# Performance work log

Hardware: AMD Instinct MI355X
Metric: run time of the kernel (lower is better)

Reference implementation:

```python
import jax, jax.numpy as jnp
import numpy as np

N_NODES = 262144          # 8192 graphs * 32 nodes
N_EDGES = 2097152         # avg degree 8
C_IN = 64
C_HID = 64
C_OUT_GCN = 64            # 'output' layer -> channel_out = 64
NODES_PER_BATCH = 32
FC_IN = NODES_PER_BATCH * C_OUT_GCN   # 2048
FC_HID = 256
OUT_DIM = 32
NEG_SLOPE = 0.2


def setup_inputs() -> dict:
    key = jax.random.key(0)
    ks = jax.random.split(key, 16)
    def glorot(k, shape):
        fan_in, fan_out = shape[0], shape[-1]
        lim = jnp.sqrt(6.0 / (fan_in + fan_out))
        return jax.random.uniform(k, shape, jnp.float32, -lim, lim)
    inp = {
        "x": jax.random.normal(ks[0], (N_NODES, C_IN), jnp.float32),
        "edge_index": jax.random.randint(ks[1], (2, N_EDGES), 0, N_NODES, jnp.int64),
        # GATConv layer 1
        "W1": glorot(ks[2], (C_IN, C_HID)),
        "att_src1": glorot(ks[3], (C_HID,)),
        "att_dst1": glorot(ks[4], (C_HID,)),
        "b1": jnp.zeros((C_HID,), jnp.float32),
        # GATConv layer 2
        "W2": glorot(ks[5], (C_HID, C_OUT_GCN)),
        "att_src2": glorot(ks[6], (C_OUT_GCN,)),
        "att_dst2": glorot(ks[7], (C_OUT_GCN,)),
        "b2": jnp.zeros((C_OUT_GCN,), jnp.float32),
        # FC head
        "Wf1": glorot(ks[8], (FC_IN, FC_HID)),
        "bf1": jnp.zeros((FC_HID,), jnp.float32),
        "Wf2": glorot(ks[9], (FC_HID, OUT_DIM)),
        "bf2": jnp.zeros((OUT_DIM,), jnp.float32),
    }
    return inp


def gat_conv(x, src, dst, W, att_src, att_dst, bias):
    """PyG GATConv, heads=1, add_self_loops=False. Message flows src -> dst."""
    h = x @ W                                  # [N, C]
    a_s = h @ att_src                          # [N]
    a_d = h @ att_dst                          # [N]
    e = a_s[src] + a_d[dst]                    # [E]
    e = jnp.where(e > 0, e, NEG_SLOPE * e)     # leaky_relu
    n = x.shape[0]
    # segment softmax over edges grouped by target node
    m = jax.ops.segment_max(e, dst, num_segments=n)
    e = jnp.exp(e - m[dst])
    s = jax.ops.segment_sum(e, dst, num_segments=n)
    alpha = e / s[dst]                         # s[dst] > 0 for every existing edge
    msg = alpha[:, None] * h[src]              # [E, C]
    out = jax.ops.segment_sum(msg, dst, num_segments=n)
    return out + bias


def reference(x, edge_index, W1, att_src1, att_dst1, b1,
              W2, att_src2, att_dst2, b2, Wf1, bf1, Wf2, bf2):
    src, dst = edge_index[0], edge_index[1]
    h = gat_conv(x, src, dst, W1, att_src1, att_dst1, b1)
    h = gat_conv(h, src, dst, W2, att_src2, att_dst2, b2)
    num_batch = h.shape[0] // NODES_PER_BATCH
    g = h.reshape(num_batch, -1)               # [B, 32*64]
    f = jax.nn.relu(g @ Wf1 + bf1)
    return f @ Wf2 + bf2                       # [B, 32]
```

## Files before the change

### kernel.cpp

```cpp
#include <hip/hip_runtime.h>
#include <stdint.h>

#define N_NODES_C 262144
#define N_EDGES_C 2097152
#define NB_C      8192
#define NEG_SLOPE_C 0.2f

#define NBKT 1024
#define NPB  256
#define CHUNK 8192
#define NBINBLK 256

typedef __attribute__((ext_vector_type(4))) float f32x4;
typedef __attribute__((ext_vector_type(8))) short short8;
typedef __attribute__((ext_vector_type(4))) unsigned short us4;
typedef unsigned int u32;

static __device__ __forceinline__ unsigned short f2bf(float f) {
    unsigned int u = __builtin_bit_cast(unsigned int, f);
    unsigned int r = (u + 0x7FFFu + ((u >> 16) & 1u)) >> 16;
    return (unsigned short)r;
}
static __device__ __forceinline__ float bf2f(unsigned short u) {
    unsigned int x = ((unsigned int)u) << 16;
    return __builtin_bit_cast(float, x);
}

__global__ void zero_u32(u32* __restrict__ p, int n) {
    int i = blockIdx.x * blockDim.x + threadIdx.x;
    int stride = gridDim.x * blockDim.x;
    for (int k = i; k < n; k += stride) p[k] = 0u;
}

__global__ void transpose_cast(const float* __restrict__ in,
                               unsigned short* __restrict__ out, int R, int Cc) {
    int i = blockIdx.x * blockDim.x + threadIdx.x;
    if (i < R * Cc) {
        int r = i / Cc, c = i % Cc;
        out[(size_t)c * R + r] = f2bf(in[i]);
    }
}

__global__ __launch_bounds__(1024) void bin_count(const int* __restrict__ dst,
                                                  u32* __restrict__ gtotal) {
    __shared__ u32 hist[NBKT];
    for (int i = threadIdx.x; i < NBKT; i += 1024) hist[i] = 0u;
    __syncthreads();
    const int e0 = blockIdx.x * CHUNK;
    for (int i = threadIdx.x; i < CHUNK; i += 1024)
        atomicAdd(&hist[((u32)dst[e0 + i]) >> 8], 1u);
    __syncthreads();
    for (int i = threadIdx.x; i < NBKT; i += 1024)
        if (hist[i]) atomicAdd(&gtotal[i], hist[i]);
}

__global__ __launch_bounds__(256) void bin_scan(const u32* __restrict__ gtotal,
                                                u32* __restrict__ cbase,
                                                u32* __restrict__ gcursor) {
    __shared__ u32 sd[256];
    const int t = threadIdx.x;
    uint4 c = ((const uint4*)gtotal)[t];
    u32 s = c.x + c.y + c.z + c.w;
    sd[t] = s;
    __syncthreads();
    for (int off = 1; off < 256; off <<= 1) {
        u32 v = (t >= off) ? sd[t - off] : 0u;
        __syncthreads();
        sd[t] += v;
        __syncthreads();
    }
    u32 ex = sd[t] - s;
    u32 b0 = ex, b1 = ex + c.x, b2 = b1 + c.y, b3 = b2 + c.z;
    cbase[t * 4 + 0] = b0; gcursor[t * 4 + 0] = b0;
    cbase[t * 4 + 1] = b1; gcursor[t * 4 + 1] = b1;
    cbase[t * 4 + 2] = b2; gcursor[t * 4 + 2] = b2;
    cbase[t * 4 + 3] = b3; gcursor[t * 4 + 3] = b3;
    if (t == 255) cbase[NBKT] = N_EDGES_C;
}

__global__ __launch_bounds__(1024) void bin_scatter(const int* __restrict__ src,
                                                    const int* __restrict__ dst,
                                                    u32* __restrict__ gcursor,
                                                    u32* __restrict__ packed) {
    __shared__ u32 hist[NBKT];
    __shared__ u32 gpos[NBKT];
    __shared__ u32 cur[NBKT];
    for (int i = threadIdx.x; i < NBKT; i += 1024) { hist[i] = 0u; cur[i] = 0u; }
    __syncthreads();
    const int e0 = blockIdx.x * CHUNK;
    for (int i = threadIdx.x; i < CHUNK; i += 1024)
        atomicAdd(&hist[((u32)dst[e0 + i]) >> 8], 1u);
    __syncthreads();
    for (int i = threadIdx.x; i < NBKT; i += 1024) {
        u32 c = hist[i];
        gpos[i] = c ? atomicAdd(&gcursor[i], c) : 0u;
    }
    __syncthreads();
    for (int i = threadIdx.x; i < CHUNK; i += 1024) {
        u32 d = (u32)dst[e0 + i];
        u32 b = d >> 8;
        u32 r = atomicAdd(&cur[b], 1u);
        packed[gpos[b] + r] = (u32)src[e0 + i] | ((d & 255u) << 18);
    }
}

__global__ __launch_bounds__(256) void csr_convert(const u32* __restrict__ cbase,
                                                   const u32* __restrict__ packed,
                                                   u32* __restrict__ row_start,
                                                   int* __restrict__ sorted_src) {
    __shared__ u32 cnt[NPB];
    __shared__ u32 pos[NPB];
    const int b = blockIdx.x;
    const u32 beg = cbase[b], end = cbase[b + 1];
    const int t = threadIdx.x;
    cnt[t] = 0u;
    __syncthreads();
    for (u32 i = beg + t; i < end; i += 256)
        atomicAdd(&cnt[packed[i] >> 18], 1u);
    __syncthreads();
    pos[t] = cnt[t];
    __syncthreads();
    for (int off = 1; off < 256; off <<= 1) {
        u32 v = (t >= off) ? pos[t - off] : 0u;
        __syncthreads();
        pos[t] += v;
        __syncthreads();
    }
    const u32 ex = pos[t] - cnt[t];
    row_start[b * NPB + t] = beg + ex;
    __syncthreads();
    cnt[t] = ex;
    __syncthreads();
    for (u32 i = beg + t; i < end; i += 256) {
        u32 p = packed[i];
        u32 r = atomicAdd(&cnt[p >> 18], 1u);
        sorted_src[beg + r] = (int)(p & 0x3FFFFu);
    }
    if (b == 0 && t == 0) row_start[N_NODES_C] = N_EDGES_C;
}

template <int LAYER>
__global__ __launch_bounds__(256) void transform_mfma(
    const void* __restrict__ xin_,
    const unsigned short* __restrict__ Wt,
    const float* __restrict__ att_s, const float* __restrict__ att_d,
    const float* __restrict__ bias_in,
    unsigned short* __restrict__ h_bf,
    float* __restrict__ a_s, float* __restrict__ a_d)
{
    const int lane = threadIdx.x & 63;
    const int wid  = threadIdx.x >> 6;
    const int col  = lane & 15;
    const int kl   = lane >> 4;

    short8 bfr[4][2];
    #pragma unroll
    for (int t = 0; t < 4; ++t)
        #pragma unroll
        for (int kh = 0; kh < 2; ++kh)
            bfr[t][kh] = *(const short8*)(Wt + (t * 16 + col) * 64 + kh * 32 + kl * 8);

    float attS[4], attD[4];
    #pragma unroll
    for (int t = 0; t < 4; ++t) {
        attS[t] = att_s[t * 16 + col];
        attD[t] = att_d[t * 16 + col];
    }
    float bofs[2][8];
    if constexpr (LAYER == 2) {
        #pragma unroll
        for (int kh = 0; kh < 2; ++kh)
            #pragma unroll
            for (int j = 0; j < 8; ++j) bofs[kh][j] = bias_in[kh * 32 + kl * 8 + j];
    }

    const int g = blockIdx.x * 4 + wid;
    const int arow = g * 16 + col;
    short8 af[2];
    if constexpr (LAYER == 1) {
        const float* xp = (const float*)xin_ + (size_t)arow * 64;
        #pragma unroll
        for (int kh = 0; kh < 2; ++kh) {
            f32x4 v0 = *(const f32x4*)(xp + kh * 32 + kl * 8);
            f32x4 v1 = *(const f32x4*)(xp + kh * 32 + kl * 8 + 4);
            short8 a;
            #pragma unroll
            for (int j = 0; j < 4; ++j) {
                a[j]     = (short)f2bf(v0[j]);
                a[4 + j] = (short)f2bf(v1[j]);
            }
            af[kh] = a;
        }
    } else {
        const unsigned short* xp = (const unsigned short*)xin_ + (size_t)arow * 64;
        #pragma unroll
        for (int kh = 0; kh < 2; ++kh) {
            short8 raw = *(const short8*)(xp + kh * 32 + kl * 8);
            short8 a;
            #pragma unroll
            for (int j = 0; j < 8; ++j)
                a[j] = (short)f2bf(bf2f((unsigned short)raw[j]) + bofs[kh][j]);
            af[kh] = a;
        }
    }

    f32x4 acc[4];
    #pragma unroll
    for (int t = 0; t < 4; ++t) {
        f32x4 d = {0.f, 0.f, 0.f, 0.f};
        d = __builtin_amdgcn_mfma_f32_16x16x32_bf16(af[0], bfr[t][0], d, 0, 0, 0);
        d = __builtin_amdgcn_mfma_f32_16x16x32_bf16(af[1], bfr[t][1], d, 0, 0, 0);
        acc[t] = d;
    }

    float ps[4] = {0.f, 0.f, 0.f, 0.f}, pd[4] = {0.f, 0.f, 0.f, 0.f};
    #pragma unroll
    for (int t = 0; t < 4; ++t) {
        #pragma unroll
        for (int j = 0; j < 4; ++j) {
            int node = g * 16 + kl * 4 + j;
            h_bf[(size_t)node * 64 + t * 16 + col] = f2bf(acc[t][j]);
            ps[j] += acc[t][j] * attS[t];
            pd[j] += acc[t][j] * attD[t];
        }
    }
    #pragma unroll
    for (int m = 1; m < 16; m <<= 1) {
        #pragma unroll
        for (int j = 0; j < 4; ++j) {
            ps[j] += __shfl_xor(ps[j], m, 64);
            pd[j] += __shfl_xor(pd[j], m, 64);
        }
    }
    if (col == 0) {
        #pragma unroll
        for (int j = 0; j < 4; ++j) {
            int node = g * 16 + kl * 4 + j;
            a_s[node] = ps[j];
            a_d[node] = pd[j];
        }
    }
}

static __device__ __forceinline__ void agg_one_node(
    int node, u32 beg, u32 end, int lane, int sub, int c4,
    const int* __restrict__ sorted_src, const float* __restrict__ a_s,
    const float* __restrict__ a_d, const unsigned short* __restrict__ h_bf,
    const float* __restrict__ bias_out, unsigned short* __restrict__ agg_bf)
{
    f32x4 acc = {0.f, 0.f, 0.f, 0.f};
    if (end > beg) {
        const float ad = a_d[node];
        float l = 0.f;
        for (u32 base = beg; base < end; base += 64) {
            u32 i = base + lane;
            bool valid = i < end;
            int s = valid ? sorted_src[i] : 0;
            float e = valid ? a_s[s] + ad : 0.f;
            e = e > 0.f ? e : NEG_SLOPE_C * e;
            float p = valid ? __expf(e) : 0.f;
            #pragma unroll
            for (int off = 32; off; off >>= 1) p += __shfl_xor(p, off, 64);
            l += p;
        }
        const float inv = 1.f / l;
        for (u32 base = beg; base < end; base += 64) {
            u32 i = base + lane;
            bool valid = i < end;
            int s = valid ? sorted_src[i] : 0;
            float e = valid ? a_s[s] + ad : 0.f;
            e = e > 0.f ? e : NEG_SLOPE_C * e;
            float p = valid ? __expf(e) * inv : 0.f;
            int c2 = (int)min(64u, end - base);
            for (int t = 0; t < c2; t += 4) {
                int j = t + sub;
                float al = __shfl(p, j, 64);
                int   sj = __shfl(s, j, 64);
                if (j >= c2) al = 0.f;
                us4 hv = *(const us4*)(h_bf + (size_t)sj * 64 + c4);
                acc[0] += al * bf2f(hv[0]);
                acc[1] += al * bf2f(hv[1]);
                acc[2] += al * bf2f(hv[2]);
                acc[3] += al * bf2f(hv[3]);
            }
        }
    }
    #pragma unroll
    for (int k = 0; k < 4; ++k) {
        acc[k] += __shfl_xor(acc[k], 16, 64);
        acc[k] += __shfl_xor(acc[k], 32, 64);
    }
    if (sub == 0) {
        us4 o;
        if (bias_out) {
            #pragma unroll
            for (int k = 0; k < 4; ++k) o[k] = f2bf(acc[k] + bias_out[c4 + k]);
        } else {
            #pragma unroll
            for (int k = 0; k < 4; ++k) o[k] = f2bf(acc[k]);
        }
        *(us4*)(agg_bf + (size_t)node * 64 + c4) = o;
    }
}

__global__ __launch_bounds__(256) void gat_aggregate(
    const u32* __restrict__ row_start, const int* __restrict__ sorted_src,
    const float* __restrict__ a_s, const float* __restrict__ a_d,
    const unsigned short* __restrict__ h_bf, const float* __restrict__ bias_out,
    unsigned short* __restrict__ agg_bf)
{
    const int lane = threadIdx.x & 63;
    const int sub  = lane >> 4;
    const int j    = lane & 15;
    const int c4   = j * 4;
    const int wid = (blockIdx.x * blockDim.x + threadIdx.x) >> 6;
    const int n0 = wid * 4;

    uint4 r4 = *(const uint4*)(row_start + n0);
    const u32 rs0 = r4.x, rs1 = r4.y, rs2 = r4.z, rs3 = r4.w;
    const u32 rs4 = row_start[n0 + 4];
    const int d0 = (int)(rs1 - rs0), d1 = (int)(rs2 - rs1);
    const int d2 = (int)(rs3 - rs2), d3 = (int)(rs4 - rs3);
    const int mx = max(max(d0, d1), max(d2, d3));
    const u32 beg = rs0, end = rs4;
    const int tot = (int)(end - beg);

    if (mx <= 16) {
        const u32 rlo = (sub == 0) ? rs0 : (sub == 1) ? rs1 : (sub == 2) ? rs2 : rs3;
        const int ck  = (sub == 0) ? d0  : (sub == 1) ? d1  : (sub == 2) ? d2  : d3;
        const bool valid = j < ck;
        int s_own = valid ? sorted_src[rlo + j] : 0;
        float e = valid ? a_s[s_own] + a_d[n0 + sub] : 0.f;
        e = e > 0.f ? e : NEG_SLOPE_C * e;
        const float p = valid ? __expf(e) : 0.f;
        float l = p;
        l += __shfl_xor(l, 1, 64);
        l += __shfl_xor(l, 2, 64);
        l += __shfl_xor(l, 4, 64);
        l += __shfl_xor(l, 8, 64);
        const float alpha = valid ? p * (1.f / l) : 0.f;

        const int base = sub * 16;
        f32x4 acc = {0.f, 0.f, 0.f, 0.f};
        for (int t = 0; t < ck; t += 2) {
            float al0 = __shfl(alpha, base + t, 64);
            int   s0  = __shfl(s_own, base + t, 64);
            float al1 = __shfl(alpha, base + t + 1, 64);
            int   s1  = __shfl(s_own, base + t + 1, 64);
            if (t + 1 >= ck) al1 = 0.f;
            us4 h0 = *(const us4*)(h_bf + (size_t)s0 * 64 + c4);
            us4 h1 = *(const us4*)(h_bf + (size_t)s1 * 64 + c4);
            acc[0] += al0 * bf2f(h0[0]) + al1 * bf2f(h1[0]);
            acc[1] += al0 * bf2f(h0[1]) + al1 * bf2f(h1[1]);
            acc[2] += al0 * bf2f(h0[2]) + al1 * bf2f(h1[2]);
            acc[3] += al0 * bf2f(h0[3]) + al1 * bf2f(h1[3]);
        }

        us4 o;
        if (bias_out) {
            #pragma unroll
            for (int q = 0; q < 4; ++q) o[q] = f2bf(acc[q] + bias_out[c4 + q]);
        } else {
            #pragma unroll
            for (int q = 0; q < 4; ++q) o[q] = f2bf(acc[q]);
        }
        *(us4*)(agg_bf + (size_t)(n0 + sub) * 64 + c4) = o;
        return;
    }

    if (tot > 64) {
        agg_one_node(n0 + 0, rs0, rs1, lane, sub, c4, sorted_src, a_s, a_d, h_bf, bias_out, agg_bf);
        agg_one_node(n0 + 1, rs1, rs2, lane, sub, c4, sorted_src, a_s, a_d, h_bf, bias_out, agg_bf);
        agg_one_node(n0 + 2, rs2, rs3, lane, sub, c4, sorted_src, a_s, a_d, h_bf, bias_out, agg_bf);
        agg_one_node(n0 + 3, rs3, rs4, lane, sub, c4, sorted_src, a_s, a_d, h_bf, bias_out, agg_bf);
        return;
    }

    const u32 i = beg + (u32)lane;
    const bool valid = i < end;
    int s = valid ? sorted_src[i] : 0;
    const u32 r1 = rs1 - beg, r2 = rs2 - beg, r3 = rs3 - beg;
    const int nid = (int)((u32)lane >= r1) + (int)((u32)lane >= r2) + (int)((u32)lane >= r3);
    float e = valid ? a_s[s] + a_d[n0 + nid] : 0.f;
    e = e > 0.f ? e : NEG_SLOPE_C * e;
    const float p = valid ? __expf(e) : 0.f;

    float l0 = (nid == 0) ? p : 0.f;
    float l1 = (nid == 1) ? p : 0.f;
    float l2 = (nid == 2) ? p : 0.f;
    float l3 = (nid == 3) ? p : 0.f;
    #pragma unroll
    for (int off = 32; off; off >>= 1) {
        l0 += __shfl_xor(l0, off, 64);
        l1 += __shfl_xor(l1, off, 64);
        l2 += __shfl_xor(l2, off, 64);
        l3 += __shfl_xor(l3, off, 64);
    }
    const float i0 = 1.f / l0, i1 = 1.f / l1, i2 = 1.f / l2, i3 = 1.f / l3;
    const float invk = (nid < 2) ? (nid == 0 ? i0 : i1) : (nid == 2 ? i2 : i3);
    const float alpha = valid ? p * invk : 0.f;

    #pragma unroll
    for (int k = 0; k < 4; ++k) {
        const u32 rloK = (k == 0) ? rs0 : (k == 1) ? rs1 : (k == 2) ? rs2 : rs3;
        const u32 rhiK = (k == 0) ? rs1 : (k == 1) ? rs2 : (k == 2) ? rs3 : rs4;
        const int rb = (int)(rloK - beg);
        const int ck = (int)(rhiK - rloK);
        f32x4 acc = {0.f, 0.f, 0.f, 0.f};
        for (int t = 0; t < ck; t += 8) {
            const int j0 = rb + t + sub;
            const int j1 = j0 + 4;
            float al0 = __shfl(alpha, j0, 64);
            int   s0  = __shfl(s, j0, 64);
            float al1 = __shfl(alpha, j1, 64);
            int   s1  = __shfl(s, j1, 64);
            if (t + sub >= ck)     al0 = 0.f;
            if (t + 4 + sub >= ck) al1 = 0.f;
            us4 h0 = *(const us4*)(h_bf + (size_t)s0 * 64 + c4);
            us4 h1 = *(const us4*)(h_bf + (size_t)s1 * 64 + c4);
            acc[0] += al0 * bf2f(h0[0]) + al1 * bf2f(h1[0]);
            acc[1] += al0 * bf2f(h0[1]) + al1 * bf2f(h1[1]);
            acc[2] += al0 * bf2f(h0[2]) + al1 * bf2f(h1[2]);
            acc[3] += al0 * bf2f(h0[3]) + al1 * bf2f(h1[3]);
        }
        #pragma unroll
        for (int q = 0; q < 4; ++q) {
            acc[q] += __shfl_xor(acc[q], 16, 64);
            acc[q] += __shfl_xor(acc[q], 32, 64);
        }
        if (sub == 0) {
            us4 o;
            if (bias_out) {
                #pragma unroll
                for (int q = 0; q < 4; ++q) o[q] = f2bf(acc[q] + bias_out[c4 + q]);
            } else {
                #pragma unroll
                for (int q = 0; q < 4; ++q) o[q] = f2bf(acc[q]);
            }
            *(us4*)(agg_bf + (size_t)(n0 + k) * 64 + c4) = o;
        }
    }
}

__global__ __launch_bounds__(512) void fc1_mfma(
    const unsigned short* __restrict__ agg_bf,
    const unsigned short* __restrict__ Wf1t,
    const float* __restrict__ bf1, float* __restrict__ fbuf)
{
    __shared__ float sh[4][64][33];
    const int lane = threadIdx.x & 63;
    const int w    = threadIdx.x >> 6;
    const int cg   = w & 3;
    const int kh   = w >> 2;
    const int col  = lane & 15;
    const int kl   = lane >> 4;
    const int rbase = blockIdx.x * 32;

    const int kbase = kh * 1024 + kl * 8;
    const unsigned short* a0p = agg_bf + (size_t)(rbase + col) * 2048 + kbase;
    const unsigned short* a1p = a0p + 16 * 2048;
    const unsigned short* bp0 = Wf1t + (size_t)(cg * 64 + col) * 2048 + kbase;
    const unsigned short* bp1 = bp0 + 16 * 2048;
    const unsigned short* bp2 = bp0 + 32 * 2048;
    const unsigned short* bp3 = bp0 + 48 * 2048;

    f32x4 acc[2][4];
    #pragma unroll
    for (int rt = 0; rt < 2; ++rt)
        #pragma unroll
        for (int ct = 0; ct < 4; ++ct) acc[rt][ct] = (f32x4){0.f, 0.f, 0.f, 0.f};

    short8 a0 = *(const short8*)a0p, a1 = *(const short8*)a1p;
    short8 b0 = *(const short8*)bp0, b1 = *(const short8*)bp1;
    short8 b2 = *(const short8*)bp2, b3 = *(const short8*)bp3;

    for (int ks = 0; ks < 32; ++ks) {
        const short8 ca0 = a0, ca1 = a1, cb0 = b0, cb1 = b1, cb2 = b2, cb3 = b3;
        if (ks < 31) {
            const int off = (ks + 1) * 32;
            a0 = *(const short8*)(a0p + off);
            a1 = *(const short8*)(a1p + off);
            b0 = *(const short8*)(bp0 + off);
            b1 = *(const short8*)(bp1 + off);
            b2 = *(const short8*)(bp2 + off);
            b3 = *(const short8*)(bp3 + off);
        }
        acc[0][0] = __builtin_amdgcn_mfma_f32_16x16x32_bf16(ca0, cb0, acc[0][0], 0, 0, 0);
        acc[1][0] = __builtin_amdgcn_mfma_f32_16x16x32_bf16(ca1, cb0, acc[1][0], 0, 0, 0);
        acc[0][1] = __builtin_amdgcn_mfma_f32_16x16x32_bf16(ca0, cb1, acc[0][1], 0, 0, 0);
        acc[1][1] = __builtin_amdgcn_mfma_f32_16x16x32_bf16(ca1, cb1, acc[1][1], 0, 0, 0);
        acc[0][2] = __builtin_amdgcn_mfma_f32_16x16x32_bf16(ca0, cb2, acc[0][2], 0, 0, 0);
        acc[1][2] = __builtin_amdgcn_mfma_f32_16x16x32_bf16(ca1, cb2, acc[1][2], 0, 0, 0);
        acc[0][3] = __builtin_amdgcn_mfma_f32_16x16x32_bf16(ca0, cb3, acc[0][3], 0, 0, 0);
        acc[1][3] = __builtin_amdgcn_mfma_f32_16x16x32_bf16(ca1, cb3, acc[1][3], 0, 0, 0);
    }

    if (kh == 1) {
        #pragma unroll
        for (int rt = 0; rt < 2; ++rt)
            #pragma unroll
            for (int ct = 0; ct < 4; ++ct)
                #pragma unroll
                for (int j = 0; j < 4; ++j)
                    sh[cg][lane][rt * 16 + ct * 4 + j] = acc[rt][ct][j];
    }
    __syncthreads();
    if (kh == 0) {
        #pragma unroll
        for (int rt = 0; rt < 2; ++rt) {
            #pragma unroll
            for (int ct = 0; ct < 4; ++ct) {
                const int ocol = cg * 64 + ct * 16 + col;
                const float bias = bf1[ocol];
                #pragma unroll
                for (int j = 0; j < 4; ++j) {
                    int row = rbase + rt * 16 + kl * 4 + j;
                    float v = acc[rt][ct][j] + sh[cg][lane][rt * 16 + ct * 4 + j] + bias;
                    fbuf[(size_t)row * 256 + ocol] = v > 0.f ? v : 0.f;
                }
            }
        }
    }
}

__global__ __launch_bounds__(256) void fc2_f32(
    const float* __restrict__ fbuf, const float* __restrict__ Wf2,
    const float* __restrict__ bf2v, float* __restrict__ out)
{
    __shared__ float w[256 * 32];
    for (int i = threadIdx.x; i < 256 * 32; i += 256) w[i] = Wf2[i];
    __syncthreads();
    int tid = blockIdx.x * 256 + threadIdx.x;
    int b = tid >> 5, o = tid & 31;
    float acc = bf2v[o];
    const float* fp = fbuf + (size_t)b * 256;
    for (int j = 0; j < 256; j += 4) {
        f32x4 f4 = *(const f32x4*)(fp + j);
        acc += f4[0] * w[(j + 0) * 32 + o];
        acc += f4[1] * w[(j + 1) * 32 + o];
        acc += f4[2] * w[(j + 2) * 32 + o];
        acc += f4[3] * w[(j + 3) * 32 + o];
    }
    out[(size_t)b * 32 + o] = acc;
}

extern "C" void kernel_launch(void* const* d_in, const int* in_sizes, int n_in,
                              void* d_out, int out_size, void* d_ws, size_t ws_size,
                              hipStream_t stream)
{
    const float* x    = (const float*)d_in[0];
    const int*   ei   = (const int*)d_in[1];
    const float* W1   = (const float*)d_in[2];
    const float* as1  = (const float*)d_in[3];
    const float* ad1  = (const float*)d_in[4];
    const float* b1   = (const float*)d_in[5];
    const float* W2   = (const float*)d_in[6];
    const float* as2  = (const float*)d_in[7];
    const float* ad2  = (const float*)d_in[8];
    const float* b2   = (const float*)d_in[9];
    const float* Wf1  = (const float*)d_in[10];
    const float* bf1  = (const float*)d_in[11];
    const float* Wf2  = (const float*)d_in[12];
    const float* bf2v = (const float*)d_in[13];

    const int* src = ei;
    const int* dst = ei + N_EDGES_C;

    char* ws = (char*)d_ws;
    unsigned short* h_bf   = (unsigned short*)ws; ws += (size_t)N_NODES_C * 64 * 2;
    unsigned short* agg_bf = (unsigned short*)ws; ws += (size_t)N_NODES_C * 64 * 2;
    float* a_s          = (float*)ws;          ws += (size_t)N_NODES_C * 4;
    float* a_d          = (float*)ws;          ws += (size_t)N_NODES_C * 4;
    u32* row_start      = (u32*)ws;            ws += (size_t)(N_NODES_C + 4) * 4;
    int* sorted_src     = (int*)ws;            ws += (size_t)N_EDGES_C * 4;
    u32* packed         = (u32*)ws;            ws += (size_t)N_EDGES_C * 4;
    u32* gtotal         = (u32*)ws;            ws += NBKT * 4;
    u32* cbase          = (u32*)ws;            ws += (NBKT + 4) * 4;
    u32* gcursor        = (u32*)ws;            ws += NBKT * 4;
    float* fbuf         = (float*)ws;          ws += (size_t)NB_C * 256 * 4;
    unsigned short* Wt1 = (unsigned short*)ws; ws += 64 * 64 * 2;
    unsigned short* Wt2 = (unsigned short*)ws; ws += 64 * 64 * 2;
    unsigned short* Wf1t = (unsigned short*)ws; ws += (size_t)256 * 2048 * 2;

    transpose_cast<<<16, 256, 0, stream>>>(W1, Wt1, 64, 64);
    transpose_cast<<<16, 256, 0, stream>>>(W2, Wt2, 64, 64);
    transpose_cast<<<2048, 256, 0, stream>>>(Wf1, Wf1t, 2048, 256);

    zero_u32<<<1, 256, 0, stream>>>(gtotal, NBKT);
    bin_count<<<NBINBLK, 1024, 0, stream>>>(dst, gtotal);
    bin_scan<<<1, 256, 0, stream>>>(gtotal, cbase, gcursor);
    bin_scatter<<<NBINBLK, 1024, 0, stream>>>(src, dst, gcursor, packed);
    csr_convert<<<NBKT, 256, 0, stream>>>(cbase, packed, row_start, sorted_src);

    transform_mfma<1><<<4096, 256, 0, stream>>>(x, Wt1, as1, ad1, nullptr, h_bf, a_s, a_d);
    gat_aggregate<<<16384, 256, 0, stream>>>(row_start, sorted_src, a_s, a_d, h_bf,
                                             nullptr, agg_bf);

    transform_mfma<2><<<4096, 256, 0, stream>>>(agg_bf, Wt2, as2, ad2, b1, h_bf, a_s, a_d);
    gat_aggregate<<<16384, 256, 0, stream>>>(row_start, sorted_src, a_s, a_d, h_bf,
                                             b2, agg_bf);

    fc1_mfma<<<256, 512, 0, stream>>>(agg_bf, Wf1t, bf1, fbuf);
    fc2_f32<<<1024, 256, 0, stream>>>(fbuf, Wf2, bf2v, (float*)d_out);
}
```

Measured before the change: 286.3 us.

## Fuse FC1 and FC2 into one head kernel; reuse per-block bin histograms

The FC2 layer is folded into the FC1 MFMA kernel. The ReLU'd hidden activations for each 32-row tile are staged in shared memory and multiplied by Wf2 directly, so the 8 MB fbuf round trip and one launch go away. Separately, bin_count now stores each block's histogram to global memory, and bin_scatter reads it back instead of re-reading dst and rebuilding the histogram with shared atomics. The fused FC2 reads Wf2 from global/L1 rather than shared memory, and only 512 threads per block do that tail work.

```diff
diff --git a/kernel.cpp b/kernel.cpp
--- a/kernel.cpp
+++ b/kernel.cpp
@@ -10,6 +10,7 @@
 #define NPB  256
 #define CHUNK 8192
 #define NBINBLK 256
+#define FSTR 260
 
 typedef __attribute__((ext_vector_type(4))) float f32x4;
 typedef __attribute__((ext_vector_type(8))) short short8;
@@ -42,7 +43,8 @@
 }
 
 __global__ __launch_bounds__(1024) void bin_count(const int* __restrict__ dst,
-                                                  u32* __restrict__ gtotal) {
+                                                  u32* __restrict__ gtotal,
+                                                  u32* __restrict__ bhist) {
     __shared__ u32 hist[NBKT];
     for (int i = threadIdx.x; i < NBKT; i += 1024) hist[i] = 0u;
     __syncthreads();
@@ -50,8 +52,11 @@
     for (int i = threadIdx.x; i < CHUNK; i += 1024)
         atomicAdd(&hist[((u32)dst[e0 + i]) >> 8], 1u);
     __syncthreads();
-    for (int i = threadIdx.x; i < NBKT; i += 1024)
-        if (hist[i]) atomicAdd(&gtotal[i], hist[i]);
+    for (int i = threadIdx.x; i < NBKT; i += 1024) {
+        u32 c = hist[i];
+        bhist[(size_t)blockIdx.x * NBKT + i] = c;
+        if (c) atomicAdd(&gtotal[i], c);
+    }
 }
 
 __global__ __launch_bounds__(256) void bin_scan(const u32* __restrict__ gtotal,
@@ -80,22 +85,18 @@
 
 __global__ __launch_bounds__(1024) void bin_scatter(const int* __restrict__ src,
                                                     const int* __restrict__ dst,
+                                                    const u32* __restrict__ bhist,
                                                     u32* __restrict__ gcursor,
                                                     u32* __restrict__ packed) {
-    __shared__ u32 hist[NBKT];
     __shared__ u32 gpos[NBKT];
     __shared__ u32 cur[NBKT];
-    for (int i = threadIdx.x; i < NBKT; i += 1024) { hist[i] = 0u; cur[i] = 0u; }
+    for (int i = threadIdx.x; i < NBKT; i += 1024) {
+        u32 c = bhist[(size_t)blockIdx.x * NBKT + i];
+        gpos[i] = c ? atomicAdd(&gcursor[i], c) : 0u;
+        cur[i] = 0u;
+    }
     __syncthreads();
     const int e0 = blockIdx.x * CHUNK;
-    for (int i = threadIdx.x; i < CHUNK; i += 1024)
-        atomicAdd(&hist[((u32)dst[e0 + i]) >> 8], 1u);
-    __syncthreads();
-    for (int i = threadIdx.x; i < NBKT; i += 1024) {
-        u32 c = hist[i];
-        gpos[i] = c ? atomicAdd(&gcursor[i], c) : 0u;
-    }
-    __syncthreads();
     for (int i = threadIdx.x; i < CHUNK; i += 1024) {
         u32 d = (u32)dst[e0 + i];
         u32 b = d >> 8;
@@ -442,12 +443,15 @@
     }
 }
 
-__global__ __launch_bounds__(512) void fc1_mfma(
+__global__ __launch_bounds__(512) void fc_head(
     const unsigned short* __restrict__ agg_bf,
     const unsigned short* __restrict__ Wf1t,
-    const float* __restrict__ bf1, float* __restrict__ fbuf)
+    const float* __restrict__ bf1,
+    const float* __restrict__ Wf2,
+    const float* __restrict__ bf2v,
+    float* __restrict__ out)
 {
-    __shared__ float sh[4][64][33];
+    __shared__ float shmem[4 * 64 * 33];
     const int lane = threadIdx.x & 63;
     const int w    = threadIdx.x >> 6;
     const int cg   = w & 3;
@@ -501,8 +505,8 @@
             #pragma unroll
             for (int ct = 0; ct < 4; ++ct)
                 #pragma unroll
-                for (int j = 0; j < 4; ++j)
-                    sh[cg][lane][rt * 16 + ct * 4 + j] = acc[rt][ct][j];
+                for (int q = 0; q < 4; ++q)
+                    shmem[cg * (64 * 33) + lane * 33 + rt * 16 + ct * 4 + q] = acc[rt][ct][q];
     }
     __syncthreads();
     if (kh == 0) {
@@ -513,35 +517,43 @@
                 const int ocol = cg * 64 + ct * 16 + col;
                 const float bias = bf1[ocol];
                 #pragma unroll
-                for (int j = 0; j < 4; ++j) {
-                    int row = rbase + rt * 16 + kl * 4 + j;
-                    float v = acc[rt][ct][j] + sh[cg][lane][rt * 16 + ct * 4 + j] + bias;
-                    fbuf[(size_t)row * 256 + ocol] = v > 0.f ? v : 0.f;
+                for (int q = 0; q < 4; ++q) {
+                    float v = acc[rt][ct][q]
+                            + shmem[cg * (64 * 33) + lane * 33 + rt * 16 + ct * 4 + q]
+                            + bias;
+                    acc[rt][ct][q] = v > 0.f ? v : 0.f;
                 }
             }
         }
     }
-}
-
-__global__ __launch_bounds__(256) void fc2_f32(
-    const float* __restrict__ fbuf, const float* __restrict__ Wf2,
-    const float* __restrict__ bf2v, float* __restrict__ out)
-{
-    __shared__ float w[256 * 32];
-    for (int i = threadIdx.x; i < 256 * 32; i += 256) w[i] = Wf2[i];
-    __syncthreads();
-    int tid = blockIdx.x * 256 + threadIdx.x;
-    int b = tid >> 5, o = tid & 31;
-    float acc = bf2v[o];
-    const float* fp = fbuf + (size_t)b * 256;
-    for (int j = 0; j < 256; j += 4) {
-        f32x4 f4 = *(const f32x4*)(fp + j);
-        acc += f4[0] * w[(j + 0) * 32 + o];
-        acc += f4[1] * w[(j + 1) * 32 + o];
-        acc += f4[2] * w[(j + 2) * 32 + o];
-        acc += f4[3] * w[(j + 3) * 32 + o];
-    }
-    out[(size_t)b * 32 + o] = acc;
+    __syncthreads();
+    if (kh == 0) {
+        #pragma unroll
+        for (int rt = 0; rt < 2; ++rt) {
+            #pragma unroll
+            for (int ct = 0; ct < 4; ++ct) {
+                const int ocol = cg * 64 + ct * 16 + col;
+                #pragma unroll
+                for (int q = 0; q < 4; ++q) {
+                    int row = rt * 16 + kl * 4 + q;
+                    shmem[row * FSTR + ocol] = acc[rt][ct][q];
+                }
+            }
+        }
+    }
+    __syncthreads();
+    for (int u = threadIdx.x; u < 1024; u += 512) {
+        const int b = u >> 5, o = u & 31;
+        float a2 = bf2v[o];
+        const float* fp = shmem + b * FSTR;
+        for (int jj = 0; jj < 256; jj += 4) {
+            a2 += fp[jj + 0] * Wf2[(jj + 0) * 32 + o];
+            a2 += fp[jj + 1] * Wf2[(jj + 1) * 32 + o];
+            a2 += fp[jj + 2] * Wf2[(jj + 2) * 32 + o];
+            a2 += fp[jj + 3] * Wf2[(jj + 3) * 32 + o];
+        }
+        out[(size_t)(rbase + b) * 32 + o] = a2;
+    }
 }
 
 extern "C" void kernel_launch(void* const* d_in, const int* in_sizes, int n_in,
@@ -574,10 +586,10 @@
     u32* row_start      = (u32*)ws;            ws += (size_t)(N_NODES_C + 4) * 4;
     int* sorted_src     = (int*)ws;            ws += (size_t)N_EDGES_C * 4;
     u32* packed         = (u32*)ws;            ws += (size_t)N_EDGES_C * 4;
+    u32* bhist          = (u32*)ws;            ws += (size_t)NBINBLK * NBKT * 4;
     u32* gtotal         = (u32*)ws;            ws += NBKT * 4;
     u32* cbase          = (u32*)ws;            ws += (NBKT + 4) * 4;
     u32* gcursor        = (u32*)ws;            ws += NBKT * 4;
-    float* fbuf         = (float*)ws;          ws += (size_t)NB_C * 256 * 4;
     unsigned short* Wt1 = (unsigned short*)ws; ws += 64 * 64 * 2;
     unsigned short* Wt2 = (unsigned short*)ws; ws += 64 * 64 * 2;
     unsigned short* Wf1t = (unsigned short*)ws; ws += (size_t)256 * 2048 * 2;
@@ -587,9 +599,9 @@
     transpose_cast<<<2048, 256, 0, stream>>>(Wf1, Wf1t, 2048, 256);
 
     zero_u32<<<1, 256, 0, stream>>>(gtotal, NBKT);
-    bin_count<<<NBINBLK, 1024, 0, stream>>>(dst, gtotal);
+    bin_count<<<NBINBLK, 1024, 0, stream>>>(dst, gtotal, bhist);
     bin_scan<<<1, 256, 0, stream>>>(gtotal, cbase, gcursor);
-    bin_scatter<<<NBINBLK, 1024, 0, stream>>>(src, dst, gcursor, packed);
+    bin_scatter<<<NBINBLK, 1024, 0, stream>>>(src, dst, bhist, gcursor, packed);
     csr_convert<<<NBKT, 256, 0, stream>>>(cbase, packed, row_start, sorted_src);
 
     transform_mfma<1><<<4096, 256, 0, stream>>>(x, Wt1, as1, ad1, nullptr, h_bf, a_s, a_d);
@@ -600,6 +612,5 @@
     gat_aggregate<<<16384, 256, 0, stream>>>(row_start, sorted_src, a_s, a_d, h_bf,
                                              b2, agg_bf);
 
-    fc1_mfma<<<256, 512, 0, stream>>>(agg_bf, Wf1t, bf1, fbuf);
-    fc2_f32<<<1024, 256, 0, stream>>>(fbuf, Wf2, bf2v, (float*)d_out);
-}
+    fc_head<<<256, 512, 0, stream>>>(agg_bf, Wf1t, bf1, Wf2, bf2v, (float*)d_out);
+}
```

New measurement: 283.3 us. No clear change (-1.1%).
